# Kernel optimization log

Hardware: AMD Instinct MI355X
Metric: run time of the kernel (lower is better)

The kernel has to match this reference:

```python
import jax, jax.numpy as jnp
import numpy as np

D_IN = 768
D_OUT = 768
NUM_HEADS = 12
HEAD_DIM = D_OUT // NUM_HEADS


def setup_inputs() -> dict:
    key = jax.random.key(0)
    ks = jax.random.split(key, 6)
    s = 1.0 / np.sqrt(D_IN)
    X = jax.random.normal(ks[0], (4, 2048, D_IN), dtype=jnp.float32)
    Wq = jax.random.uniform(ks[1], (D_IN, D_OUT), jnp.float32, -s, s)
    Wk = jax.random.uniform(ks[2], (D_IN, D_OUT), jnp.float32, -s, s)
    Wv = jax.random.uniform(ks[3], (D_IN, D_OUT), jnp.float32, -s, s)
    Wo = jax.random.uniform(ks[4], (D_OUT, D_OUT), jnp.float32, -s, s)
    bo = jax.random.uniform(ks[5], (D_OUT,), jnp.float32, -s, s)
    return {"X": X, "Wq": Wq, "Wk": Wk, "Wv": Wv, "Wo": Wo, "bo": bo}


def reference(X, Wq, Wk, Wv, Wo, bo):
    b, n, _ = X.shape
    # QKV projections, split heads -> [b, h, n, d]
    def split(t):
        return t.reshape(b, n, NUM_HEADS, HEAD_DIM).transpose(0, 2, 1, 3)
    q = split(X @ Wq)
    k = split(X @ Wk)
    v = split(X @ Wv)
    scores = jnp.einsum('bhqd,bhkd->bhqk', q, k) / np.sqrt(HEAD_DIM).astype(np.float32)
    causal = jnp.triu(jnp.ones((n, n), dtype=bool), k=1)
    scores = jnp.where(causal, -jnp.inf, scores)
    attn = jax.nn.softmax(scores, axis=-1)  # dropout p=0 -> identity
    ctx = jnp.einsum('bhqk,bhkd->bhqd', attn, v)
    ctx = ctx.transpose(0, 2, 1, 3).reshape(b, n, D_OUT)
    return ctx @ Wo + bo
```

## Files before the change

### kernel.cpp

```cpp
#include <hip/hip_runtime.h>
#include <stdint.h>

#define B_  4
#define N_  2048
#define D_  768
#define H_  12
#define HD_ 64
#define M_  (B_*N_)

typedef short bf8 __attribute__((ext_vector_type(8)));
typedef float f32x4 __attribute__((ext_vector_type(4)));

static __device__ __forceinline__ unsigned short f2bf(float f) {
    unsigned u = __float_as_uint(f);
    unsigned r = u + 0x7fffu + ((u >> 16) & 1u);
    return (unsigned short)(r >> 16);
}

static __device__ __forceinline__ unsigned pk2bf(float f0, float f1) {
    return ((__float_as_uint(f1) + 0x8000u) & 0xFFFF0000u) |
           ((__float_as_uint(f0) + 0x8000u) >> 16);
}

#if __has_builtin(__builtin_amdgcn_exp2f)
#define EXP2(x) __builtin_amdgcn_exp2f(x)
#else
#define EXP2(x) exp2f(x)
#endif

#define GLOAD_LDS16(gptr, lptr)                                                   \
    __builtin_amdgcn_global_load_lds(                                             \
        (const __attribute__((address_space(1))) void*)(gptr),                    \
        (__attribute__((address_space(3))) void*)(lptr), 16, 0, 0)

#define QSCALE 0.1803368801111204f

__global__ __launch_bounds__(256) void convert_x(const float* __restrict__ X,
                                                 unsigned short* __restrict__ Xb) {
    const size_t i = ((size_t)blockIdx.x * 256 + threadIdx.x) * 8;
    const float4 a = *(const float4*)(X + i);
    const float4 b = *(const float4*)(X + i + 4);
    ushort4 lo, hi;
    lo.x = f2bf(a.x); lo.y = f2bf(a.y); lo.z = f2bf(a.z); lo.w = f2bf(a.w);
    hi.x = f2bf(b.x); hi.y = f2bf(b.y); hi.z = f2bf(b.z); hi.w = f2bf(b.w);
    *(ushort4*)(Xb + i)     = lo;
    *(ushort4*)(Xb + i + 4) = hi;
}

__global__ __launch_bounds__(256) void transpose_w(
    const float* __restrict__ Wq, const float* __restrict__ Wk,
    const float* __restrict__ Wv, const float* __restrict__ Wo,
    unsigned short* __restrict__ Wqt, unsigned short* __restrict__ Wkt,
    unsigned short* __restrict__ Wvt, unsigned short* __restrict__ Wot)
{
    __shared__ float tile[32][33];
    const int z = blockIdx.z;
    const float* W = (z == 0) ? Wq : (z == 1) ? Wk : (z == 2) ? Wv : Wo;
    unsigned short* Wt = (z == 0) ? Wqt : (z == 1) ? Wkt : (z == 2) ? Wvt : Wot;
    const int k0 = blockIdx.x * 32, n0 = blockIdx.y * 32;
    const int tx = threadIdx.x & 31, ty = threadIdx.x >> 5;
    #pragma unroll
    for (int i = 0; i < 4; ++i)
        tile[ty + 8 * i][tx] = W[(size_t)(k0 + ty + 8 * i) * D_ + n0 + tx];
    __syncthreads();
    #pragma unroll
    for (int i = 0; i < 4; ++i)
        Wt[(size_t)(n0 + ty + 8 * i) * D_ + k0 + tx] = f2bf(tile[tx][ty + 8 * i]);
}

__global__ __launch_bounds__(256) void qkv_mfma(
    const unsigned short* __restrict__ Xb,
    const unsigned short* __restrict__ Wqt, const unsigned short* __restrict__ Wkt,
    const unsigned short* __restrict__ Wvt,
    unsigned short* __restrict__ Qb, unsigned short* __restrict__ Kb,
    unsigned short* __restrict__ Vt)
{
    __shared__ unsigned short As[8192];
    __shared__ unsigned short Bs[8192];

    const int t = threadIdx.x;
    const int wave = t >> 6, lane = t & 63;
    const int col = lane & 15, quad = lane >> 4;
    const int wm = (wave & 1) * 64, wn = (wave >> 1) * 64;

    const int m0 = blockIdx.x * 128;
    const int n0 = blockIdx.y * 128;
    const int mat = blockIdx.z;
    const unsigned short* Wt = (mat == 0) ? Wqt : (mat == 1) ? Wkt : Wvt;
    const bool sw = (mat != 2);

    const unsigned short* Ag = Xb + (size_t)(m0 + (t >> 2)) * D_ + (t & 3) * 8;
    const unsigned short* Bg = Wt + (size_t)(n0 + (t >> 2)) * D_ + (t & 3) * 8;
    unsigned short* AsD = As + t * 8;
    unsigned short* BsD = Bs + t * 8;

    f32x4 acc[4][4] = {};

    for (int k0 = 0; k0 < D_; k0 += 64) {
        __syncthreads();
        GLOAD_LDS16(Ag + k0,                        AsD);
        GLOAD_LDS16(Ag + k0 + 32,                   AsD + 4096);
        GLOAD_LDS16(Ag + (size_t)64 * D_ + k0,      AsD + 2048);
        GLOAD_LDS16(Ag + (size_t)64 * D_ + k0 + 32, AsD + 6144);
        GLOAD_LDS16(Bg + k0,                        BsD);
        GLOAD_LDS16(Bg + k0 + 32,                   BsD + 4096);
        GLOAD_LDS16(Bg + (size_t)64 * D_ + k0,      BsD + 2048);
        GLOAD_LDS16(Bg + (size_t)64 * D_ + k0 + 32, BsD + 6144);
        __syncthreads();

        #pragma unroll
        for (int ks = 0; ks < 2; ++ks) {
            bf8 a[4], b[4];
            #pragma unroll
            for (int i = 0; i < 4; ++i)
                a[i] = *(const bf8*)(As + ks * 4096 + (wm + i * 16 + col) * 32 + quad * 8);
            #pragma unroll
            for (int j = 0; j < 4; ++j)
                b[j] = *(const bf8*)(Bs + ks * 4096 + (wn + j * 16 + col) * 32 + quad * 8);
            if (sw) {
                #pragma unroll
                for (int i = 0; i < 4; ++i)
                    #pragma unroll
                    for (int j = 0; j < 4; ++j)
                        acc[i][j] = __builtin_amdgcn_mfma_f32_16x16x32_bf16(b[j], a[i], acc[i][j], 0, 0, 0);
            } else {
                #pragma unroll
                for (int i = 0; i < 4; ++i)
                    #pragma unroll
                    for (int j = 0; j < 4; ++j)
                        acc[i][j] = __builtin_amdgcn_mfma_f32_16x16x32_bf16(a[i], b[j], acc[i][j], 0, 0, 0);
            }
        }
    }

    if (sw) {
        unsigned short* Out = (mat == 0) ? Qb : Kb;
        const float qsc = (mat == 0) ? QSCALE : 1.0f;
        #pragma unroll
        for (int i = 0; i < 4; ++i) {
            const int token = m0 + wm + i * 16 + col;
            const int bb = token >> 11, nn = token & (N_ - 1);
            #pragma unroll
            for (int j = 0; j < 4; ++j) {
                const int n = n0 + wn + j * 16 + quad * 4;
                const int h = n >> 6, d = n & 63;
                ushort4 pk;
                pk.x = f2bf(acc[i][j][0] * qsc);
                pk.y = f2bf(acc[i][j][1] * qsc);
                pk.z = f2bf(acc[i][j][2] * qsc);
                pk.w = f2bf(acc[i][j][3] * qsc);
                *(ushort4*)(Out + ((size_t)(bb * H_ + h) * N_ + nn) * HD_ + d) = pk;
            }
        }
    } else {
        #pragma unroll
        for (int j = 0; j < 4; ++j) {
            const int n = n0 + wn + j * 16 + col;
            const int h = n >> 6, d = n & 63;
            #pragma unroll
            for (int i = 0; i < 4; ++i) {
                const int mb = m0 + wm + i * 16 + quad * 4;
                const int bb = mb >> 11, nn = mb & (N_ - 1);
                ushort4 pk;
                pk.x = f2bf(acc[i][j][0]); pk.y = f2bf(acc[i][j][1]);
                pk.z = f2bf(acc[i][j][2]); pk.w = f2bf(acc[i][j][3]);
                *(ushort4*)(Vt + ((size_t)(bb * H_ + h) * HD_ + d) * N_ + nn) = pk;
            }
        }
    }
}

#define PS 72

static __device__ __forceinline__ void qk_softmax(
    const bf8 (&ka)[4][2], bf8 qb0, bf8 qb1,
    int k0, int q, bool mask, float& lpart,
    unsigned short* Pw, int col, int quad)
{
    f32x4 s[4] = {};
    __builtin_amdgcn_s_setprio(1);
    #pragma unroll
    for (int kc = 0; kc < 4; ++kc) {
        s[kc] = __builtin_amdgcn_mfma_f32_16x16x32_bf16(ka[kc][0], qb0, s[kc], 0, 0, 0);
        s[kc] = __builtin_amdgcn_mfma_f32_16x16x32_bf16(ka[kc][1], qb1, s[kc], 0, 0, 0);
    }
    __builtin_amdgcn_s_setprio(0);

    float p[4][4];
    if (mask) {
        #pragma unroll
        for (int kc = 0; kc < 4; ++kc)
            #pragma unroll
            for (int r = 0; r < 4; ++r) {
                const int key = k0 + kc * 16 + quad * 4 + r;
                p[kc][r] = EXP2((key > q) ? -INFINITY : s[kc][r]);
            }
    } else {
        #pragma unroll
        for (int kc = 0; kc < 4; ++kc)
            #pragma unroll
            for (int r = 0; r < 4; ++r) p[kc][r] = EXP2(s[kc][r]);
    }

    #pragma unroll
    for (int kc = 0; kc < 4; ++kc)
        #pragma unroll
        for (int r = 0; r < 4; ++r) lpart += p[kc][r];

    #pragma unroll
    for (int kc = 0; kc < 4; ++kc) {
        uint2 pk;
        pk.x = pk2bf(p[kc][0], p[kc][1]);
        pk.y = pk2bf(p[kc][2], p[kc][3]);
        *(uint2*)(Pw + col * PS + kc * 16 + quad * 4) = pk;
    }
}

static __device__ __forceinline__ void pv_acc(
    const unsigned short* Pw, const bf8 (&va)[4][2],
    f32x4 (&o)[4], int col, int quad)
{
    const bf8 pb0 = *(const bf8*)(Pw + col * PS + quad * 8);
    const bf8 pb1 = *(const bf8*)(Pw + col * PS + 32 + quad * 8);
    __builtin_amdgcn_s_setprio(1);
    #pragma unroll
    for (int dc = 0; dc < 4; ++dc) {
        o[dc] = __builtin_amdgcn_mfma_f32_16x16x32_bf16(va[dc][0], pb0, o[dc], 0, 0, 0);
        o[dc] = __builtin_amdgcn_mfma_f32_16x16x32_bf16(va[dc][1], pb1, o[dc], 0, 0, 0);
    }
    __builtin_amdgcn_s_setprio(0);
}

__global__ __launch_bounds__(256, 3) void attn_mfma(
    const unsigned short* __restrict__ Qb,
    const unsigned short* __restrict__ Kb,
    const unsigned short* __restrict__ Vt,
    unsigned short* __restrict__ Ctxb)
{
    __shared__ unsigned short Kl[2][64 * PS];
    __shared__ unsigned short Vl[2][64 * PS];
    __shared__ unsigned short Pl[4][16 * PS];

    const int t = threadIdx.x;
    const int wave = t >> 6;
    const int lane = t & 63;
    const int col  = lane & 15;
    const int quad = lane >> 4;

    const int bid = blockIdx.x;
    const int bh  = bid >> 4;
    const int x   = bid & 15;
    const int tl  = x, th = 31 - x;
    const int q0L = tl * 64 + wave * 16;
    const int q0H = th * 64 + wave * 16;
    const int qL  = q0L + col;
    const int qH  = q0H + col;

    const unsigned short* Kp = Kb + (size_t)bh * N_ * HD_;
    const unsigned short* Vp = Vt + (size_t)bh * HD_ * N_;
    const unsigned short* QpL = Qb + ((size_t)bh * N_ + q0L) * HD_;
    const unsigned short* QpH = Qb + ((size_t)bh * N_ + q0H) * HD_;

    const bf8 qbL0 = *(const bf8*)(QpL + (size_t)col * HD_ + quad * 8);
    const bf8 qbL1 = *(const bf8*)(QpL + (size_t)col * HD_ + 32 + quad * 8);
    const bf8 qbH0 = *(const bf8*)(QpH + (size_t)col * HD_ + quad * 8);
    const bf8 qbH1 = *(const bf8*)(QpH + (size_t)col * HD_ + 32 + quad * 8);

    f32x4 oL[4] = {}, oH[4] = {};
    float lL = 0.f, lH = 0.f;

    unsigned short* Pw = &Pl[wave][0];

    const int srow = t >> 3;
    const int scol = (t & 7) * 8;
    const unsigned short* Kg = Kp + (size_t)srow * HD_ + scol;
    const unsigned short* Vg = Vp + (size_t)srow * N_ + scol;
    const int kO0 = srow * PS + scol;
    const int kO1 = (srow + 32) * PS + scol;

    const int iters = 32 - x;

    uint4 kr0 = *(const uint4*)(Kg);
    uint4 kr1 = *(const uint4*)(Kg + (size_t)32 * HD_);
    uint4 vr0 = *(const uint4*)(Vg);
    uint4 vr1 = *(const uint4*)(Vg + (size_t)32 * N_);
    *(uint4*)(Kl[0] + kO0) = kr0;
    *(uint4*)(Kl[0] + kO1) = kr1;
    *(uint4*)(Vl[0] + kO0) = vr0;
    *(uint4*)(Vl[0] + kO1) = vr1;
    kr0 = *(const uint4*)(Kg + (size_t)64 * HD_);
    kr1 = *(const uint4*)(Kg + (size_t)96 * HD_);
    vr0 = *(const uint4*)(Vg + 64);
    vr1 = *(const uint4*)(Vg + (size_t)32 * N_ + 64);

    for (int kt = 0; kt < iters; ++kt) {
        const int k0 = kt * 64;
        const bool actL = (kt <= tl);
        const unsigned short* Kc = Kl[kt & 1];
        const unsigned short* Vc = Vl[kt & 1];
        unsigned short* Kn = Kl[(kt + 1) & 1];
        unsigned short* Vn = Vl[(kt + 1) & 1];

        __syncthreads();

        if (kt + 1 < iters) {
            *(uint4*)(Kn + kO0) = kr0;
            *(uint4*)(Kn + kO1) = kr1;
            *(uint4*)(Vn + kO0) = vr0;
            *(uint4*)(Vn + kO1) = vr1;
        }
        if (kt + 2 < iters) {
            const size_t k2 = (size_t)(kt + 2) * 64;
            kr0 = *(const uint4*)(Kg + k2 * HD_);
            kr1 = *(const uint4*)(Kg + (k2 + 32) * HD_);
            vr0 = *(const uint4*)(Vg + k2);
            vr1 = *(const uint4*)(Vg + (size_t)32 * N_ + k2);
        }

        bf8 ka[4][2];
        #pragma unroll
        for (int kc = 0; kc < 4; ++kc) {
            ka[kc][0] = *(const bf8*)(Kc + (kc * 16 + col) * PS + quad * 8);
            ka[kc][1] = *(const bf8*)(Kc + (kc * 16 + col) * PS + 32 + quad * 8);
        }

        qk_softmax(ka, qbH0, qbH1, k0, qH, kt == th, lH, Pw, col, quad);

        bf8 va[4][2];
        #pragma unroll
        for (int dc = 0; dc < 4; ++dc) {
            va[dc][0] = *(const bf8*)(Vc + (dc * 16 + col) * PS + quad * 8);
            va[dc][1] = *(const bf8*)(Vc + (dc * 16 + col) * PS + 32 + quad * 8);
        }

        pv_acc(Pw, va, oH, col, quad);

        if (actL) {
            qk_softmax(ka, qbL0, qbL1, k0, qL, kt == tl, lL, Pw, col, quad);
            pv_acc(Pw, va, oL, col, quad);
        }
    }

    const int b = bh / H_;
    const int h = bh % H_;
    {
        float l = lH;
        l += __shfl_xor(l, 16, 64);
        l += __shfl_xor(l, 32, 64);
        const float inv = 1.0f / l;
        unsigned short* cp = Ctxb + ((size_t)(b * N_ + qH)) * D_ + h * HD_;
        #pragma unroll
        for (int dc = 0; dc < 4; ++dc) {
            uint2 pk;
            pk.x = pk2bf(oH[dc][0] * inv, oH[dc][1] * inv);
            pk.y = pk2bf(oH[dc][2] * inv, oH[dc][3] * inv);
            *(uint2*)(cp + dc * 16 + quad * 4) = pk;
        }
    }
    {
        float l = lL;
        l += __shfl_xor(l, 16, 64);
        l += __shfl_xor(l, 32, 64);
        const float inv = 1.0f / l;
        unsigned short* cp = Ctxb + ((size_t)(b * N_ + qL)) * D_ + h * HD_;
        #pragma unroll
        for (int dc = 0; dc < 4; ++dc) {
            uint2 pk;
            pk.x = pk2bf(oL[dc][0] * inv, oL[dc][1] * inv);
            pk.y = pk2bf(oL[dc][2] * inv, oL[dc][3] * inv);
            *(uint2*)(cp + dc * 16 + quad * 4) = pk;
        }
    }
}

__global__ __launch_bounds__(256) void out_mfma(
    const unsigned short* __restrict__ Ctxb,
    const unsigned short* __restrict__ Wot,
    const float* __restrict__ bo,
    float* __restrict__ Out)
{
    __shared__ unsigned short As[8192];
    __shared__ unsigned short Bs[8192];

    const int t = threadIdx.x;
    const int wave = t >> 6, lane = t & 63;
    const int col = lane & 15, quad = lane >> 4;
    const int wm = (wave & 1) * 64, wn = (wave >> 1) * 64;

    const int m0 = blockIdx.x * 128;
    const int n0 = blockIdx.y * 128;

    const unsigned short* Ag = Ctxb + (size_t)(m0 + (t >> 2)) * D_ + (t & 3) * 8;
    const unsigned short* Bg = Wot + (size_t)(n0 + (t >> 2)) * D_ + (t & 3) * 8;
    unsigned short* AsD = As + t * 8;
    unsigned short* BsD = Bs + t * 8;

    f32x4 acc[4][4] = {};

    for (int k0 = 0; k0 < D_; k0 += 64) {
        __syncthreads();
        GLOAD_LDS16(Ag + k0,                        AsD);
        GLOAD_LDS16(Ag + k0 + 32,                   AsD + 4096);
        GLOAD_LDS16(Ag + (size_t)64 * D_ + k0,      AsD + 2048);
        GLOAD_LDS16(Ag + (size_t)64 * D_ + k0 + 32, AsD + 6144);
        GLOAD_LDS16(Bg + k0,                        BsD);
        GLOAD_LDS16(Bg + k0 + 32,                   BsD + 4096);
        GLOAD_LDS16(Bg + (size_t)64 * D_ + k0,      BsD + 2048);
        GLOAD_LDS16(Bg + (size_t)64 * D_ + k0 + 32, BsD + 6144);
        __syncthreads();

        #pragma unroll
        for (int ks = 0; ks < 2; ++ks) {
            bf8 a[4], b[4];
            #pragma unroll
            for (int i = 0; i < 4; ++i)
                a[i] = *(const bf8*)(As + ks * 4096 + (wm + i * 16 + col) * 32 + quad * 8);
            #pragma unroll
            for (int j = 0; j < 4; ++j)
                b[j] = *(const bf8*)(Bs + ks * 4096 + (wn + j * 16 + col) * 32 + quad * 8);
            #pragma unroll
            for (int i = 0; i < 4; ++i)
                #pragma unroll
                for (int j = 0; j < 4; ++j)
                    acc[i][j] = __builtin_amdgcn_mfma_f32_16x16x32_bf16(b[j], a[i], acc[i][j], 0, 0, 0);
        }
    }

    #pragma unroll
    for (int i = 0; i < 4; ++i) {
        const int m = m0 + wm + i * 16 + col;
        #pragma unroll
        for (int j = 0; j < 4; ++j) {
            const int n = n0 + wn + j * 16 + quad * 4;
            const float4 bias = *(const float4*)(bo + n);
            float4 o;
            o.x = acc[i][j][0] + bias.x;
            o.y = acc[i][j][1] + bias.y;
            o.z = acc[i][j][2] + bias.z;
            o.w = acc[i][j][3] + bias.w;
            *(float4*)(Out + (size_t)m * D_ + n) = o;
        }
    }
}

extern "C" void kernel_launch(void* const* d_in, const int* in_sizes, int n_in,
                              void* d_out, int out_size, void* d_ws, size_t ws_size,
                              hipStream_t stream) {
    const float* X  = (const float*)d_in[0];
    const float* Wq = (const float*)d_in[1];
    const float* Wk = (const float*)d_in[2];
    const float* Wv = (const float*)d_in[3];
    const float* Wo = (const float*)d_in[4];
    const float* bo = (const float*)d_in[5];
    float* out = (float*)d_out;

    const size_t elems = (size_t)M_ * D_;
    const size_t welems = (size_t)D_ * D_;
    unsigned short* Xb  = (unsigned short*)d_ws;
    unsigned short* Wqt = Xb + elems;
    unsigned short* Wkt = Wqt + welems;
    unsigned short* Wvt = Wkt + welems;
    unsigned short* Wot = Wvt + welems;
    unsigned short* Qb  = Wot + welems;
    unsigned short* Kb  = Qb + elems;
    unsigned short* Vt  = Kb + elems;
    unsigned short* Ctxb = Xb;

    convert_x<<<dim3(elems / 2048), 256, 0, stream>>>(X, Xb);
    transpose_w<<<dim3(24, 24, 4), 256, 0, stream>>>(Wq, Wk, Wv, Wo, Wqt, Wkt, Wvt, Wot);

    qkv_mfma<<<dim3(M_ / 128, D_ / 128, 3), 256, 0, stream>>>(Xb, Wqt, Wkt, Wvt, Qb, Kb, Vt);

    attn_mfma<<<dim3(B_ * H_ * 16), 256, 0, stream>>>(Qb, Kb, Vt, Ctxb);

    out_mfma<<<dim3(M_ / 128, D_ / 128), 256, 0, stream>>>(Ctxb, Wot, bo, out);
}
```

Measured before the change: 212.5 us.

## Keep softmax probabilities in registers by permuting V loads to match MFMA layout

The probability tile P no longer goes through LDS. The QK^T MFMA output fragments are packed directly into the B-operand registers for the PV MFMA. To keep the reduction index consistent, V is read from LDS as four 4-element chunks per lane, laid out to match the permuted key ordering. This removes the per-wave P shared buffer, its LDS write and read, and the implicit dependency on them. Occupancy is raised from 3 to 4 blocks per CU through launch bounds, at the cost of narrower LDS reads for V and more register pressure.

```diff
diff --git a/kernel.cpp b/kernel.cpp
--- a/kernel.cpp
+++ b/kernel.cpp
@@ -175,7 +175,7 @@
 static __device__ __forceinline__ void qk_softmax(
     const bf8 (&ka)[4][2], bf8 qb0, bf8 qb1,
     int k0, int q, bool mask, float& lpart,
-    unsigned short* Pw, int col, int quad)
+    bf8& pb0, bf8& pb1, int quad)
 {
     f32x4 s[4] = {};
     __builtin_amdgcn_s_setprio(1);
@@ -207,21 +207,18 @@
         #pragma unroll
         for (int r = 0; r < 4; ++r) lpart += p[kc][r];
 
-    #pragma unroll
-    for (int kc = 0; kc < 4; ++kc) {
-        uint2 pk;
-        pk.x = pk2bf(p[kc][0], p[kc][1]);
-        pk.y = pk2bf(p[kc][2], p[kc][3]);
-        *(uint2*)(Pw + col * PS + kc * 16 + quad * 4) = pk;
-    }
+    uint4 u0, u1;
+    u0.x = pk2bf(p[0][0], p[0][1]); u0.y = pk2bf(p[0][2], p[0][3]);
+    u0.z = pk2bf(p[1][0], p[1][1]); u0.w = pk2bf(p[1][2], p[1][3]);
+    u1.x = pk2bf(p[2][0], p[2][1]); u1.y = pk2bf(p[2][2], p[2][3]);
+    u1.z = pk2bf(p[3][0], p[3][1]); u1.w = pk2bf(p[3][2], p[3][3]);
+    pb0 = *(bf8*)&u0;
+    pb1 = *(bf8*)&u1;
 }
 
 static __device__ __forceinline__ void pv_acc(
-    const unsigned short* Pw, const bf8 (&va)[4][2],
-    f32x4 (&o)[4], int col, int quad)
-{
-    const bf8 pb0 = *(const bf8*)(Pw + col * PS + quad * 8);
-    const bf8 pb1 = *(const bf8*)(Pw + col * PS + 32 + quad * 8);
+    bf8 pb0, bf8 pb1, const bf8 (&va)[4][2], f32x4 (&o)[4])
+{
     __builtin_amdgcn_s_setprio(1);
     #pragma unroll
     for (int dc = 0; dc < 4; ++dc) {
@@ -231,7 +228,7 @@
     __builtin_amdgcn_s_setprio(0);
 }
 
-__global__ __launch_bounds__(256, 3) void attn_mfma(
+__global__ __launch_bounds__(256, 4) void attn_mfma(
     const unsigned short* __restrict__ Qb,
     const unsigned short* __restrict__ Kb,
     const unsigned short* __restrict__ Vt,
@@ -239,7 +236,6 @@
 {
     __shared__ unsigned short Kl[2][64 * PS];
     __shared__ unsigned short Vl[2][64 * PS];
-    __shared__ unsigned short Pl[4][16 * PS];
 
     const int t = threadIdx.x;
     const int wave = t >> 6;
@@ -268,8 +264,6 @@
 
     f32x4 oL[4] = {}, oH[4] = {};
     float lL = 0.f, lH = 0.f;
-
-    unsigned short* Pw = &Pl[wave][0];
 
     const int srow = t >> 3;
     const int scol = (t & 7) * 8;
@@ -324,20 +318,28 @@
             ka[kc][1] = *(const bf8*)(Kc + (kc * 16 + col) * PS + 32 + quad * 8);
         }
 
-        qk_softmax(ka, qbH0, qbH1, k0, qH, kt == th, lH, Pw, col, quad);
-
         bf8 va[4][2];
         #pragma unroll
         for (int dc = 0; dc < 4; ++dc) {
-            va[dc][0] = *(const bf8*)(Vc + (dc * 16 + col) * PS + quad * 8);
-            va[dc][1] = *(const bf8*)(Vc + (dc * 16 + col) * PS + 32 + quad * 8);
-        }
-
-        pv_acc(Pw, va, oH, col, quad);
+            const unsigned short* Vrow = Vc + (dc * 16 + col) * PS;
+            const uint2 c0 = *(const uint2*)(Vrow + quad * 4);
+            const uint2 c1 = *(const uint2*)(Vrow + 16 + quad * 4);
+            const uint2 c2 = *(const uint2*)(Vrow + 32 + quad * 4);
+            const uint2 c3 = *(const uint2*)(Vrow + 48 + quad * 4);
+            uint4 u0; u0.x = c0.x; u0.y = c0.y; u0.z = c1.x; u0.w = c1.y;
+            uint4 u1; u1.x = c2.x; u1.y = c2.y; u1.z = c3.x; u1.w = c3.y;
+            va[dc][0] = *(const bf8*)&u0;
+            va[dc][1] = *(const bf8*)&u1;
+        }
+
+        bf8 pbH0, pbH1;
+        qk_softmax(ka, qbH0, qbH1, k0, qH, kt == th, lH, pbH0, pbH1, quad);
+        pv_acc(pbH0, pbH1, va, oH);
 
         if (actL) {
-            qk_softmax(ka, qbL0, qbL1, k0, qL, kt == tl, lL, Pw, col, quad);
-            pv_acc(Pw, va, oL, col, quad);
+            bf8 pbL0, pbL1;
+            qk_softmax(ka, qbL0, qbL1, k0, qL, kt == tl, lL, pbL0, pbL1, quad);
+            pv_acc(pbL0, pbL1, va, oL);
         }
     }
 
```

Result: slower. 339.3 us (+59.6%).
